# Kernel optimization log

Measured on AMD Instinct MI355X. Metric: run time of the kernel, lower is better.

The kernel has to match this reference:

```python
import jax, jax.numpy as jnp
import numpy as np

B, S, D, H, R, P = 4, 8192, 512, 8, 64, 4
HD = D // H  # 64
EPS = 1e-6


def _sketch_p4(z, G1, G2):
    # sketchwithnegativity(z, 2): M1 = M2 = z
    inv_sqrt_r = 1.0 / np.sqrt(R).astype(np.float32)
    half = inv_sqrt_r * ((z @ G1) * (z @ G2))  # [B,H,S,R]
    return half * half  # sketch(): half * half for p=4


def setup_inputs() -> dict:
    key = jax.random.key(0)
    ks = jax.random.split(key, 16)
    lin = lambda k: jax.random.normal(k, (D, D), jnp.float32) * (1.0 / np.sqrt(D))
    g = lambda k: jax.random.normal(k, (HD, R), jnp.float32) * (1.0 / np.sqrt(R))
    return {
        "x": jax.random.normal(ks[0], (B, S, D), jnp.float32),
        "Wq": lin(ks[1]), "bq": jnp.zeros((D,), jnp.float32),
        "Wk": lin(ks[2]), "bk": jnp.zeros((D,), jnp.float32),
        "Wv": lin(ks[3]), "bv": jnp.zeros((D,), jnp.float32),
        "Wp": lin(ks[4]), "bp": jnp.zeros((D,), jnp.float32),
        "gamma_q": jnp.ones((1,), jnp.float32), "beta_q": jnp.zeros((1,), jnp.float32),
        "gamma_k": jnp.ones((1,), jnp.float32), "beta_k": jnp.zeros((1,), jnp.float32),
        "qG1": g(ks[5]), "qG2": g(ks[6]),
        "kG1": g(ks[7]), "kG2": g(ks[8]),
    }


def reference(x, Wq, bq, Wk, bk, Wv, bv, Wp, bp,
              gamma_q, beta_q, gamma_k, beta_k, qG1, qG2, kG1, kG2):
    b, s, d = x.shape
    split = lambda t: t.reshape(b, s, H, HD).transpose(0, 2, 1, 3)  # [B,H,S,HD]
    q = split(x @ Wq + bq)
    k = split(x @ Wk + bk)
    v = split(x @ Wv + bv)
    q = gamma_q * q + beta_q
    k = gamma_k * k + beta_k
    phi_q = _sketch_p4(q, qG1, qG2)  # [B,H,S,R]
    phi_k = _sketch_p4(k, kG1, kG2)  # [B,H,S,R]
    # linear-attention form of attn = (phi_q phi_k^T) / rowsum; avoids [S,S]
    kv = jnp.einsum('bhsr,bhsd->bhrd', phi_k, v)          # [B,H,R,HD]
    ksum = phi_k.sum(axis=2)                              # [B,H,R]
    num = jnp.einsum('bhqr,bhrd->bhqd', phi_q, kv)        # [B,H,S,HD]
    den = jnp.einsum('bhqr,bhr->bhq', phi_q, ksum) + EPS  # [B,H,S]
    out = num / den[..., None]
    out = out.transpose(0, 2, 1, 3).reshape(b, s, d)
    return out @ Wp + bp
```

## Files before the change

kernel.cpp:

```cpp
#include <hip/hip_runtime.h>
#include <hip/hip_bf16.h>


#define SEQ 8192

typedef __attribute__((ext_vector_type(8))) short bf16x8;
typedef __attribute__((ext_vector_type(4))) float f32x4;

__device__ __forceinline__ unsigned short f2b(float f) {
    union { float f; unsigned int i; } v; v.f = f;
    unsigned int r = v.i + 0x7fffu + ((v.i >> 16) & 1u);
    return (unsigned short)(r >> 16);
}
__device__ __forceinline__ float b2f(unsigned short u) {
    union { unsigned int i; float f; } v; v.i = ((unsigned int)u) << 16; return v.f;
}

#if __has_builtin(__builtin_amdgcn_global_load_lds)
#define ASYNC_CP 1
#endif

__device__ __forceinline__ void cp16(const unsigned short* g, unsigned short* l) {
#ifdef ASYNC_CP
    __builtin_amdgcn_global_load_lds(
        (const __attribute__((address_space(1))) unsigned int*)g,
        (__attribute__((address_space(3))) unsigned int*)l, 16, 0, 0);
#endif
}

__global__ __launch_bounds__(256) void prep_all(
    const float* __restrict__ x, unsigned short* __restrict__ xb,
    const float* __restrict__ Wv, const float* __restrict__ Wp,
    unsigned short* __restrict__ WTf, unsigned short* __restrict__ WTp,
    const float* __restrict__ Wq, const float* __restrict__ bq,
    const float* __restrict__ Wk, const float* __restrict__ bk,
    const float* __restrict__ bv,
    const float* __restrict__ gq, const float* __restrict__ bbq,
    const float* __restrict__ gk, const float* __restrict__ bbk,
    const float* __restrict__ qG1, const float* __restrict__ qG2,
    const float* __restrict__ kG1, const float* __restrict__ kG2,
    float* __restrict__ cvec)
{
    const int blk = blockIdx.x;
    const int tid = threadIdx.x;

    if (blk < 8192) {
        size_t i = ((size_t)blk * 256 + tid) * 8;
        float4 a = *(const float4*)&x[i];
        float4 b = *(const float4*)&x[i + 4];
        ushort4 o1 = { f2b(a.x), f2b(a.y), f2b(a.z), f2b(a.w) };
        ushort4 o2 = { f2b(b.x), f2b(b.y), f2b(b.z), f2b(b.w) };
        *(ushort4*)&xb[i]     = o1;
        *(ushort4*)&xb[i + 4] = o2;
        return;
    }

    if (blk < 8704) {
        const int idx = blk - 8192;
        const int z = idx >> 8;
        const float* W = (z == 0) ? Wv : Wp;
        unsigned short* O = (z == 0) ? (WTf + (size_t)2048 * 512) : WTp;
        __shared__ float t[32][33];
        const int tx = tid & 31, ty = tid >> 5;
        const int k0 = ((idx >> 4) & 15) * 32, n0 = (idx & 15) * 32;
        #pragma unroll
        for (int i = 0; i < 4; ++i)
            t[ty + 8 * i][tx] = W[(size_t)(k0 + ty + 8 * i) * 512 + n0 + tx];
        __syncthreads();
        #pragma unroll
        for (int i = 0; i < 4; ++i)
            O[(size_t)(n0 + ty + 8 * i) * 512 + k0 + tx] = f2b(t[tx][ty + 8 * i]);
        return;
    }

    const int idx = blk - 8704;
    if (idx == 512) {
        for (int i = tid; i < 512; i += 256) cvec[2048 + i] = bv[i];
        return;
    }
    const int bi = idx & 31, ky = idx >> 5;
    const int zz = bi >> 4, h = (bi >> 1) & 7, p = bi & 1;
    const float* W    = zz ? Wk : Wq;
    const float* bias = zz ? bk : bq;
    const float* G    = zz ? (p ? kG2 : kG1) : (p ? qG2 : qG1);
    const float  gamma = zz ? gk[0] : gq[0];
    const float  beta  = zz ? bbk[0] : bbq[0];

    __shared__ float Gs[64][65];
    for (int i = tid; i < 4096; i += 256) Gs[i >> 6][i & 63] = G[i];
    __syncthreads();

    const int rr = tid & 63, kg = tid >> 6;
    const int jc = zz * 1024 + h * 128 + rr * 2 + p;
    const int k0 = ky * 32;
    for (int k = k0 + kg; k < k0 + 32; k += 4) {
        float s = 0.f;
        const float* wrow = &W[(size_t)k * 512 + h * 64];
        #pragma unroll 8
        for (int j = 0; j < 64; ++j) s = fmaf(wrow[j], Gs[j][rr], s);
        WTf[(size_t)jc * 512 + k] = f2b(gamma * s);
    }
    if (kg == 0 && ky == 0) {
        float cb = 0.f, cg = 0.f;
        #pragma unroll 8
        for (int j = 0; j < 64; ++j) {
            cb = fmaf(bias[h * 64 + j], Gs[j][rr], cb);
            cg += Gs[j][rr];
        }
        cvec[jc] = gamma * cb + beta * cg;
    }
}

#define STAGE_T(kk, dA, dB)                                                     \
    do {                                                                        \
        cp16(gA + (kk), dA);                                                    \
        cp16(gA + 16 * 512 + (kk), dA + 16 * 32);                               \
        cp16(gB + (kk), dB);                                                    \
        cp16(gB + 16 * 512 + (kk), dB + 16 * 32);                               \
    } while (0)

#define COMPUTE_T(SA, SB)                                                       \
    do {                                                                        \
        bf16x8 af[4], bfr[4];                                                   \
        _Pragma("unroll")                                                       \
        for (int i = 0; i < 4; ++i) {                                           \
            af[i]  = *(const bf16x8*)&(SA)[(wr * 64 + i * 16 + (lane & 15)) * 32 + cr]; \
            bfr[i] = *(const bf16x8*)&(SB)[(wc * 64 + i * 16 + (lane & 15)) * 32 + cr]; \
        }                                                                       \
        _Pragma("unroll")                                                       \
        for (int mi = 0; mi < 4; ++mi)                                          \
            _Pragma("unroll")                                                   \
            for (int ni = 0; ni < 4; ++ni)                                      \
                acc[mi][ni] = __builtin_amdgcn_mfma_f32_16x16x32_bf16(          \
                    af[mi], bfr[ni], acc[mi][ni], 0, 0, 0);                     \
    } while (0)

__global__ __launch_bounds__(256) void gemm_mfma_fused(
    const unsigned short* __restrict__ xb,
    const unsigned short* __restrict__ WTf,
    const float* __restrict__ cvec,
    unsigned short* __restrict__ PHIQ, unsigned short* __restrict__ PHIKT,
    unsigned short* __restrict__ VT)
{
    __shared__ __align__(16) unsigned short As[2][128 * 32];
    __shared__ __align__(16) unsigned short Bs[2][128 * 32];

    const int tid = threadIdx.x;
    const int w = tid >> 6, lane = tid & 63;
    const int flat = blockIdx.x;
    const int xcd = flat & 7, slot = flat >> 3;
    const int n0 = (xcd * 32 + slot / 20) * 128;
    const int j0 = (slot % 20) * 128;
    const int wr = w >> 1, wc = w & 1;

    const int r0 = w * 32 + (lane >> 2);
    const int kq = (lane & 3) * 8;
    const unsigned short* gA = &xb[(size_t)(n0 + r0) * 512 + kq];
    const unsigned short* gB = &WTf[(size_t)(j0 + r0) * 512 + kq];
    unsigned short* lA0 = &As[0][(w * 32) * 32];
    unsigned short* lA1 = &As[1][(w * 32) * 32];
    unsigned short* lB0 = &Bs[0][(w * 32) * 32];
    unsigned short* lB1 = &Bs[1][(w * 32) * 32];

    f32x4 acc[4][4];
    #pragma unroll
    for (int i = 0; i < 4; ++i)
        #pragma unroll
        for (int j = 0; j < 4; ++j) { acc[i][j] = (f32x4){0.f, 0.f, 0.f, 0.f}; }

    const int cr = (lane >> 4) * 8;

    STAGE_T(0, lA0, lB0);
    __syncthreads();

    #pragma unroll 1
    for (int tt = 0; tt < 16; tt += 2) {
        STAGE_T((tt + 1) * 32, lA1, lB1);
        COMPUTE_T(As[0], Bs[0]);
        __syncthreads();
        if (tt + 2 < 16) STAGE_T((tt + 2) * 32, lA0, lB0);
        COMPUTE_T(As[1], Bs[1]);
        __syncthreads();
    }

    const int bq = n0 >> 13;
    const int sq = n0 & (SEQ - 1);
    const int t0 = sq + wr * 64 + (lane >> 4) * 4;

    if (j0 < 2048) {
        const int zq = j0 >> 10;
        const int h  = (j0 >> 7) & 7;
        #pragma unroll
        for (int ni = 0; ni < 4; ++ni) {
            const int loc = wc * 64 + ni * 16 + (lane & 15);
            const float cv = cvec[j0 + loc];
            const int rr = loc >> 1;
            #pragma unroll
            for (int mi = 0; mi < 4; ++mi) {
                float ph[4];
                #pragma unroll
                for (int r = 0; r < 4; ++r) {
                    float u = acc[mi][ni][r] + cv;
                    float up = __shfl_xor(u, 1);
                    float hh = 0.125f * u * up;
                    ph[r] = hh * hh;
                }
                if ((lane & 1) == 0) {
                    if (zq == 0) {
                        #pragma unroll
                        for (int r = 0; r < 4; ++r)
                            PHIQ[((size_t)(bq * 8 + h) * SEQ + t0 + mi * 16 + r) * 64 + rr]
                                = f2b(ph[r]);
                    } else {
                        ushort4 o = { f2b(ph[0]), f2b(ph[1]), f2b(ph[2]), f2b(ph[3]) };
                        *(ushort4*)&PHIKT[((size_t)((bq * 8 + h) * 64 + rr)) * SEQ
                                          + t0 + mi * 16] = o;
                    }
                }
            }
        }
    } else {
        #pragma unroll
        for (int ni = 0; ni < 4; ++ni) {
            const int loc = wc * 64 + ni * 16 + (lane & 15);
            const int n = (j0 - 2048) + loc;
            const float cv = cvec[j0 + loc];
            #pragma unroll
            for (int mi = 0; mi < 4; ++mi) {
                ushort4 o = { f2b(acc[mi][ni][0] + cv), f2b(acc[mi][ni][1] + cv),
                              f2b(acc[mi][ni][2] + cv), f2b(acc[mi][ni][3] + cv) };
                *(ushort4*)&VT[((size_t)(bq * 512 + n)) * SEQ + t0 + mi * 16] = o;
            }
        }
    }
}

__global__ __launch_bounds__(256) void gemm_mfma_final(
    const unsigned short* __restrict__ Ab,
    const unsigned short* __restrict__ WTp,
    const float* __restrict__ bias, float* __restrict__ out)
{
    __shared__ __align__(16) unsigned short As[2][128 * 32];
    __shared__ __align__(16) unsigned short Bs[2][128 * 32];

    const int tid = threadIdx.x;
    const int w = tid >> 6, lane = tid & 63;
    const int flat = blockIdx.x;
    const int xcd = flat & 7, slot = flat >> 3;
    const int n0 = (xcd * 32 + (slot >> 2)) * 128;
    const int j0 = (slot & 3) * 128;
    const int wr = w >> 1, wc = w & 1;

    const int r0 = w * 32 + (lane >> 2);
    const int kq = (lane & 3) * 8;
    const unsigned short* gA = &Ab[(size_t)(n0 + r0) * 512 + kq];
    const unsigned short* gB = &WTp[(size_t)(j0 + r0) * 512 + kq];
    unsigned short* lA0 = &As[0][(w * 32) * 32];
    unsigned short* lA1 = &As[1][(w * 32) * 32];
    unsigned short* lB0 = &Bs[0][(w * 32) * 32];
    unsigned short* lB1 = &Bs[1][(w * 32) * 32];

    f32x4 acc[4][4];
    #pragma unroll
    for (int i = 0; i < 4; ++i)
        #pragma unroll
        for (int j = 0; j < 4; ++j) { acc[i][j] = (f32x4){0.f, 0.f, 0.f, 0.f}; }

    const int cr = (lane >> 4) * 8;

    STAGE_T(0, lA0, lB0);
    __syncthreads();

    #pragma unroll 1
    for (int tt = 0; tt < 16; tt += 2) {
        STAGE_T((tt + 1) * 32, lA1, lB1);
        COMPUTE_T(As[0], Bs[0]);
        __syncthreads();
        if (tt + 2 < 16) STAGE_T((tt + 2) * 32, lA0, lB0);
        COMPUTE_T(As[1], Bs[1]);
        __syncthreads();
    }

    #pragma unroll
    for (int ni = 0; ni < 4; ++ni) {
        const int jcol = j0 + wc * 64 + ni * 16 + (lane & 15);
        const float bvv = bias[jcol];
        #pragma unroll
        for (int mi = 0; mi < 4; ++mi) {
            #pragma unroll
            for (int r = 0; r < 4; ++r) {
                const int t = n0 + wr * 64 + mi * 16 + (lane >> 4) * 4 + r;
                out[(size_t)t * 512 + jcol] = acc[mi][ni][r] + bvv;
            }
        }
    }
}

__global__ __launch_bounds__(256) void kv_mfma(
    const unsigned short* __restrict__ PHIKT, const unsigned short* __restrict__ VT,
    float* __restrict__ KVP, float* __restrict__ KSP)
{
    const int bh = blockIdx.x, seg = blockIdx.y;
    const int tid = threadIdx.x;
    const int w = tid >> 6, lane = tid & 63;
    const size_t pbase =
        ((size_t)bh * 64 + w * 16 + (lane & 15)) * SEQ + seg * 256 + (lane >> 4) * 8;
    const size_t vbase =
        ((size_t)((bh >> 3) * 512 + (bh & 7) * 64 + (lane & 15))) * SEQ
        + seg * 256 + (lane >> 4) * 8;

    f32x4 acc[4], ks;
    #pragma unroll
    for (int nt = 0; nt < 4; ++nt) acc[nt] = (f32x4){0.f, 0.f, 0.f, 0.f};
    ks = (f32x4){0.f, 0.f, 0.f, 0.f};
    bf16x8 ones;
    #pragma unroll
    for (int i = 0; i < 8; ++i) ones[i] = (short)0x3f80;

    #pragma unroll 2
    for (int k = 0; k < 256; k += 32) {
        bf16x8 a = *(const bf16x8*)&PHIKT[pbase + k];
        ks = __builtin_amdgcn_mfma_f32_16x16x32_bf16(a, ones, ks, 0, 0, 0);
        #pragma unroll
        for (int nt = 0; nt < 4; ++nt) {
            bf16x8 bb = *(const bf16x8*)&VT[vbase + (size_t)nt * 16 * SEQ + k];
            acc[nt] = __builtin_amdgcn_mfma_f32_16x16x32_bf16(a, bb, acc[nt], 0, 0, 0);
        }
    }

    float* kvp = &KVP[((size_t)bh * 32 + seg) * 4096];
    #pragma unroll
    for (int nt = 0; nt < 4; ++nt) {
        float4 o = { acc[nt][0], acc[nt][1], acc[nt][2], acc[nt][3] };
        *(float4*)&kvp[(nt * 16 + (lane & 15)) * 64 + w * 16 + (lane >> 4) * 4] = o;
    }
    if ((lane & 15) == 0) {
        float4 o = { ks[0], ks[1], ks[2], ks[3] };
        *(float4*)&KSP[((size_t)bh * 32 + seg) * 64 + w * 16 + (lane >> 4) * 4] = o;
    }
}

__global__ __launch_bounds__(256) void kv_reduce(
    const float* __restrict__ KVP, const float* __restrict__ KSP,
    float* __restrict__ KV, float* __restrict__ KS)
{
    const int bh = blockIdx.x;
    const int e0 = blockIdx.y * 512;
    for (int e = e0 + threadIdx.x; e < e0 + 512; e += 256) {
        float s = 0.f;
        #pragma unroll 8
        for (int c = 0; c < 32; ++c) s += KVP[(size_t)(bh * 32 + c) * 4096 + e];
        KV[(size_t)bh * 4096 + e] = s;
    }
    if (blockIdx.y == 0 && threadIdx.x < 64) {
        float s = 0.f;
        for (int c = 0; c < 32; ++c) s += KSP[(bh * 32 + c) * 64 + threadIdx.x];
        KS[bh * 64 + threadIdx.x] = s;
    }
}

__global__ __launch_bounds__(256) void attn_mfma(
    const unsigned short* __restrict__ PHIQ, const float* __restrict__ KV,
    const float* __restrict__ KS, unsigned short* __restrict__ OAb)
{
    __shared__ __align__(16) unsigned short bpad[144 * 72];
    const int bh = blockIdx.x, st = blockIdx.y;
    const int tid = threadIdx.x;
    const int b = bh >> 3, h = bh & 7;

    for (int i = tid; i < 144 * 64; i += 256) {
        const int n = i >> 6, r = i & 63;
        float val;
        if (n < 64)        val = KV[(size_t)bh * 4096 + n * 64 + r];
        else if (n < 128)  { float x = KV[(size_t)bh * 4096 + (n - 64) * 64 + r];
                             val = x - b2f(f2b(x)); }
        else if (n == 128) val = KS[bh * 64 + r];
        else if (n == 129) { float x = KS[bh * 64 + r]; val = x - b2f(f2b(x)); }
        else               val = 0.f;
        bpad[n * 72 + r] = f2b(val);
    }
    __syncthreads();

    const int w = tid >> 6, lane = tid & 63;
    bf16x8 bf[9][2];
    #pragma unroll
    for (int nt = 0; nt < 9; ++nt) {
        const unsigned short* bp = &bpad[(nt * 16 + (lane & 15)) * 72 + (lane >> 4) * 8];
        bf[nt][0] = *(const bf16x8*)bp;
        bf[nt][1] = *(const bf16x8*)(bp + 32);
    }

    const int tw = st * 256 + w * 64;
    #pragma unroll
    for (int mt = 0; mt < 4; ++mt) {
        const unsigned short* ap =
            &PHIQ[((size_t)bh * SEQ + tw + mt * 16 + (lane & 15)) * 64 + (lane >> 4) * 8];
        bf16x8 a0 = *(const bf16x8*)ap;
        bf16x8 a1 = *(const bf16x8*)(ap + 32);
        f32x4 acc[9];
        #pragma unroll
        for (int nt = 0; nt < 9; ++nt) acc[nt] = (f32x4){0.f, 0.f, 0.f, 0.f};
        #pragma unroll
        for (int nt = 0; nt < 9; ++nt) {
            acc[nt] = __builtin_amdgcn_mfma_f32_16x16x32_bf16(a0, bf[nt][0], acc[nt], 0, 0, 0);
            acc[nt] = __builtin_amdgcn_mfma_f32_16x16x32_bf16(a1, bf[nt][1], acc[nt], 0, 0, 0);
        }
        #pragma unroll
        for (int r4 = 0; r4 < 4; ++r4) {
            const float den = __shfl(acc[8][r4], (lane & 48)) +
                              __shfl(acc[8][r4], (lane & 48) + 1) + 1e-6f;
            const float inv = 1.0f / den;
            const int s = tw + mt * 16 + (lane >> 4) * 4 + r4;
            #pragma unroll
            for (int nt = 0; nt < 4; ++nt)
                OAb[((size_t)b * SEQ + s) * 512 + h * 64 + nt * 16 + (lane & 15)] =
                    f2b((acc[nt][r4] + acc[nt + 4][r4]) * inv);
        }
    }
}

extern "C" void kernel_launch(void* const* d_in, const int* in_sizes, int n_in,
                              void* d_out, int out_size, void* d_ws, size_t ws_size,
                              hipStream_t stream)
{
    (void)in_sizes; (void)n_in; (void)out_size; (void)ws_size;
    const float* x   = (const float*)d_in[0];
    const float* Wq  = (const float*)d_in[1];
    const float* bq  = (const float*)d_in[2];
    const float* Wk  = (const float*)d_in[3];
    const float* bk  = (const float*)d_in[4];
    const float* Wv  = (const float*)d_in[5];
    const float* bv  = (const float*)d_in[6];
    const float* Wp  = (const float*)d_in[7];
    const float* bp  = (const float*)d_in[8];
    const float* gq  = (const float*)d_in[9];
    const float* bbq = (const float*)d_in[10];
    const float* gk  = (const float*)d_in[11];
    const float* bbk = (const float*)d_in[12];
    const float* qG1 = (const float*)d_in[13];
    const float* qG2 = (const float*)d_in[14];
    const float* kG1 = (const float*)d_in[15];
    const float* kG2 = (const float*)d_in[16];

    unsigned short* PHIQ  = (unsigned short*)d_ws;
    unsigned short* PHIKT = PHIQ + 16777216;
    unsigned short* VT    = PHIKT + 16777216;
    unsigned short* xb    = VT   + 16777216;
    unsigned short* OAb   = xb   + 16777216;
    unsigned short* WTf   = OAb  + 16777216;
    unsigned short* WTp   = WTf  + 2560 * 512;
    float* cvec = (float*)(WTp + 262144);
    float* KVP  = cvec + 2560;
    float* KSP  = KVP + 4194304;
    float* KV   = KSP + 65536;
    float* KS   = KV + 131072;
    float* out  = (float*)d_out;

    hipLaunchKernelGGL(prep_all, dim3(9217), dim3(256), 0, stream,
                       x, xb, Wv, Wp, WTf, WTp,
                       Wq, bq, Wk, bk, bv, gq, bbq, gk, bbk,
                       qG1, qG2, kG1, kG2, cvec);
    hipLaunchKernelGGL(gemm_mfma_fused, dim3(5120), dim3(256), 0, stream,
                       xb, WTf, cvec, PHIQ, PHIKT, VT);
    hipLaunchKernelGGL(kv_mfma, dim3(32, 32), dim3(256), 0, stream,
                       PHIKT, VT, KVP, KSP);
    hipLaunchKernelGGL(kv_reduce, dim3(32, 8), dim3(256), 0, stream, KVP, KSP, KV, KS);
    hipLaunchKernelGGL(attn_mfma, dim3(32, 32), dim3(256), 0, stream,
                       PHIQ, KV, KS, OAb);
    hipLaunchKernelGGL(gemm_mfma_final, dim3(1024), dim3(256), 0, stream,
                       OAb, WTp, bp, out);
}
```

Baseline: 425.9 us.

## Triple-buffer GEMM k-loop with explicit vmcnt waits and MFMA priority

Replaces the double-buffered LDS staging in both MFMA GEMM kernels with a three-stage ring buffer. Loads are kept two tiles ahead, and the loop waits with explicit s_waitcnt vmcnt counts plus raw s_barrier instead of __syncthreads draining all outstanding loads. MFMA sections are wrapped in s_setprio to favour the math waves. The aim is to overlap global-to-LDS copies with compute. In exchange it uses 48KB of LDS per block instead of 32KB, which may reduce occupancy, and it relies on vmcnt accounting for the async LDS loads being correct.

```diff
diff --git a/kernel.cpp b/kernel.cpp
--- a/kernel.cpp
+++ b/kernel.cpp
@@ -27,6 +27,9 @@
         (__attribute__((address_space(3))) unsigned int*)l, 16, 0, 0);
 #endif
 }
+
+#define SBAR      asm volatile("s_barrier" ::: "memory")
+#define WAITV(n)  asm volatile("s_waitcnt vmcnt(" #n ")" ::: "memory")
 
 __global__ __launch_bounds__(256) void prep_all(
     const float* __restrict__ x, unsigned short* __restrict__ xb,
@@ -111,28 +114,54 @@
     }
 }
 
-#define STAGE_T(kk, dA, dB)                                                     \
+#define STAGE_P(kk, off)                                                        \
     do {                                                                        \
+        unsigned short* dA = sm + (off) + (w * 32) * 32;                        \
         cp16(gA + (kk), dA);                                                    \
         cp16(gA + 16 * 512 + (kk), dA + 16 * 32);                               \
+        unsigned short* dB = sm + (off) + 4096 + (w * 32) * 32;                 \
         cp16(gB + (kk), dB);                                                    \
         cp16(gB + 16 * 512 + (kk), dB + 16 * 32);                               \
     } while (0)
 
-#define COMPUTE_T(SA, SB)                                                       \
+#define COMPUTE_P(off)                                                          \
     do {                                                                        \
         bf16x8 af[4], bfr[4];                                                   \
         _Pragma("unroll")                                                       \
         for (int i = 0; i < 4; ++i) {                                           \
-            af[i]  = *(const bf16x8*)&(SA)[(wr * 64 + i * 16 + (lane & 15)) * 32 + cr]; \
-            bfr[i] = *(const bf16x8*)&(SB)[(wc * 64 + i * 16 + (lane & 15)) * 32 + cr]; \
+            af[i]  = *(const bf16x8*)&sm[(off) + (wr * 64 + i * 16 + (lane & 15)) * 32 + cr]; \
+            bfr[i] = *(const bf16x8*)&sm[(off) + 4096 + (wc * 64 + i * 16 + (lane & 15)) * 32 + cr]; \
         }                                                                       \
+        __builtin_amdgcn_s_setprio(1);                                          \
         _Pragma("unroll")                                                       \
         for (int mi = 0; mi < 4; ++mi)                                          \
             _Pragma("unroll")                                                   \
             for (int ni = 0; ni < 4; ++ni)                                      \
                 acc[mi][ni] = __builtin_amdgcn_mfma_f32_16x16x32_bf16(          \
                     af[mi], bfr[ni], acc[mi][ni], 0, 0, 0);                     \
+        __builtin_amdgcn_s_setprio(0);                                          \
+    } while (0)
+
+#define KLOOP_P                                                                 \
+    do {                                                                        \
+        STAGE_P(0, 0u);                                                         \
+        STAGE_P(32, 8192u);                                                     \
+        unsigned o0 = 0u, o1 = 8192u, o2 = 16384u;                              \
+        _Pragma("unroll 1")                                                     \
+        for (int t = 0; t < 16; ++t) {                                          \
+            SBAR;                               \
+            if (t < 14) {                                                       \
+                STAGE_P((t + 2) * 32, o2);                                      \
+                WAITV(8);                       \
+            } else if (t == 14) {                                               \
+                WAITV(4);                                                       \
+            } else {                                                            \
+                WAITV(0);                                                       \
+            }                                                                   \
+            SBAR;                               \
+            COMPUTE_P(o0);                                                      \
+            unsigned tmp = o0; o0 = o1; o1 = o2; o2 = tmp;                      \
+        }                                                                       \
     } while (0)
 
 __global__ __launch_bounds__(256) void gemm_mfma_fused(
@@ -142,8 +171,8 @@
     unsigned short* __restrict__ PHIQ, unsigned short* __restrict__ PHIKT,
     unsigned short* __restrict__ VT)
 {
-    __shared__ __align__(16) unsigned short As[2][128 * 32];
-    __shared__ __align__(16) unsigned short Bs[2][128 * 32];
+    __shared__ __align__(16) unsigned short smem[24576];
+    unsigned short* sm = smem;
 
     const int tid = threadIdx.x;
     const int w = tid >> 6, lane = tid & 63;
@@ -157,10 +186,6 @@
     const int kq = (lane & 3) * 8;
     const unsigned short* gA = &xb[(size_t)(n0 + r0) * 512 + kq];
     const unsigned short* gB = &WTf[(size_t)(j0 + r0) * 512 + kq];
-    unsigned short* lA0 = &As[0][(w * 32) * 32];
-    unsigned short* lA1 = &As[1][(w * 32) * 32];
-    unsigned short* lB0 = &Bs[0][(w * 32) * 32];
-    unsigned short* lB1 = &Bs[1][(w * 32) * 32];
 
     f32x4 acc[4][4];
     #pragma unroll
@@ -170,18 +195,7 @@
 
     const int cr = (lane >> 4) * 8;
 
-    STAGE_T(0, lA0, lB0);
-    __syncthreads();
-
-    #pragma unroll 1
-    for (int tt = 0; tt < 16; tt += 2) {
-        STAGE_T((tt + 1) * 32, lA1, lB1);
-        COMPUTE_T(As[0], Bs[0]);
-        __syncthreads();
-        if (tt + 2 < 16) STAGE_T((tt + 2) * 32, lA0, lB0);
-        COMPUTE_T(As[1], Bs[1]);
-        __syncthreads();
-    }
+    KLOOP_P;
 
     const int bq = n0 >> 13;
     const int sq = n0 & (SEQ - 1);
@@ -240,8 +254,8 @@
     const unsigned short* __restrict__ WTp,
     const float* __restrict__ bias, float* __restrict__ out)
 {
-    __shared__ __align__(16) unsigned short As[2][128 * 32];
-    __shared__ __align__(16) unsigned short Bs[2][128 * 32];
+    __shared__ __align__(16) unsigned short smem[24576];
+    unsigned short* sm = smem;
 
     const int tid = threadIdx.x;
     const int w = tid >> 6, lane = tid & 63;
@@ -255,10 +269,6 @@
     const int kq = (lane & 3) * 8;
     const unsigned short* gA = &Ab[(size_t)(n0 + r0) * 512 + kq];
     const unsigned short* gB = &WTp[(size_t)(j0 + r0) * 512 + kq];
-    unsigned short* lA0 = &As[0][(w * 32) * 32];
-    unsigned short* lA1 = &As[1][(w * 32) * 32];
-    unsigned short* lB0 = &Bs[0][(w * 32) * 32];
-    unsigned short* lB1 = &Bs[1][(w * 32) * 32];
 
     f32x4 acc[4][4];
     #pragma unroll
@@ -268,18 +278,7 @@
 
     const int cr = (lane >> 4) * 8;
 
-    STAGE_T(0, lA0, lB0);
-    __syncthreads();
-
-    #pragma unroll 1
-    for (int tt = 0; tt < 16; tt += 2) {
-        STAGE_T((tt + 1) * 32, lA1, lB1);
-        COMPUTE_T(As[0], Bs[0]);
-        __syncthreads();
-        if (tt + 2 < 16) STAGE_T((tt + 2) * 32, lA0, lB0);
-        COMPUTE_T(As[1], Bs[1]);
-        __syncthreads();
-    }
+    KLOOP_P;
 
     #pragma unroll
     for (int ni = 0; ni < 4; ++ni) {
```

Measured after the change: 390.0 us. -8.4%, faster.
